# Performance work log

Hardware: AMD Instinct MI355X
Metric: run time of the kernel (lower is better)

The kernel has to match this reference:

```python
import jax, jax.numpy as jnp
import numpy as np

B, L, T = 32, 512, 400
EMB, PRE, ENC, ARNN, DRNN, NSYM = 512, 256, 512, 1024, 1024, 256
MEAN_COEFF, SCALE_COEFF = 1.0, 10.0


def setup_inputs() -> dict:
    key = jax.random.key(0)
    ks = jax.random.split(key, 20)
    s = 0.02
    inp = {
        'memory': jax.random.normal(ks[0], (B, L, ENC), jnp.float32),
        'decoder_inputs': jax.random.normal(ks[1], (B, EMB, T), jnp.float32),
        'memory_lengths': jax.random.randint(ks[2], (B,), L // 2, L + 1).astype(jnp.int64),
        # prenet
        'pW1': jax.random.normal(ks[3], (PRE, EMB), jnp.float32) * s,
        'pb1': jnp.zeros((PRE,), jnp.float32),
        'pW2': jax.random.normal(ks[4], (PRE, PRE), jnp.float32) * s,
        'pb2': jnp.zeros((PRE,), jnp.float32),
        # attention LSTMCell
        'aWih': jax.random.normal(ks[5], (4 * ARNN, PRE + ENC), jnp.float32) * s,
        'aWhh': jax.random.normal(ks[6], (4 * ARNN, ARNN), jnp.float32) * s,
        'abih': jnp.zeros((4 * ARNN,), jnp.float32),
        'abhh': jnp.zeros((4 * ARNN,), jnp.float32),
        # Gaussian attention param linear (weight zero-init in torch; small here)
        'attWp': jax.random.normal(ks[7], (2, ARNN), jnp.float32) * 0.001,
        'attbp': jnp.zeros((2,), jnp.float32),
        # decoder LSTMCell
        'dWih': jax.random.normal(ks[8], (4 * DRNN, ARNN + ENC), jnp.float32) * s,
        'dWhh': jax.random.normal(ks[9], (4 * DRNN, DRNN), jnp.float32) * s,
        'dbih': jnp.zeros((4 * DRNN,), jnp.float32),
        'dbhh': jnp.zeros((4 * DRNN,), jnp.float32),
        # output linear
        'oW': jax.random.normal(ks[10], (NSYM, DRNN + ENC), jnp.float32) * s,
        'ob': jnp.zeros((NSYM,), jnp.float32),
    }
    return inp


def _lstm_cell(x, h, c, Wih, Whh, bih, bhh):
    g = x @ Wih.T + bih + h @ Whh.T + bhh
    i, f, gg, o = jnp.split(g, 4, axis=-1)
    c = jax.nn.sigmoid(f) * c + jax.nn.sigmoid(i) * jnp.tanh(gg)
    h = jax.nn.sigmoid(o) * jnp.tanh(c)
    return h, c


def _decoder_core(memory, decoder_inputs, memory_lengths,
                  pW1, pb1, pW2, pb2,
                  aWih, aWhh, abih, abhh,
                  attWp, attbp,
                  dWih, dWhh, dbih, dbhh,
                  oW, ob):
    b = memory.shape[0]
    Lm = memory.shape[1]
    # go frame + time-major inputs -> prenet (dropout is identity in eval)
    x = jnp.transpose(decoder_inputs, (2, 0, 1))            # [T, B, EMB]
    x = jnp.concatenate([jnp.zeros((1, b, EMB), x.dtype), x], axis=0)  # [T+1, B, EMB]
    x = jax.nn.relu(x @ pW1.T + pb1)
    x = jax.nn.relu(x @ pW2.T + pb2)                        # [T+1, B, PRE]
    x = x[:T]                                               # loop runs T steps

    lin = jnp.arange(Lm, dtype=memory.dtype)[None, :]       # [1, L]
    pad_mask = lin >= memory_lengths[:, None].astype(memory.dtype)  # [B, L] True at pad

    def step(carry, x_t):
        ah, ac, dh, dc, ctx, mean = carry
        cell_in = jnp.concatenate([x_t, ctx], axis=1)
        ah, ac = _lstm_cell(cell_in, ah, ac, aWih, aWhh, abih, abhh)
        params = ah @ attWp.T + attbp                       # [B, 2]
        mean = mean + jnp.exp(params[:, 0:1]) * MEAN_COEFF  # [B, 1]
        scale = jnp.exp(params[:, 1:2]) * SCALE_COEFF       # [B, 1]
        Z = jnp.sqrt(2.0 * np.pi * scale ** 2)
        w = jnp.exp(-0.5 * (lin - mean) ** 2 / scale ** 2) / Z  # [B, L]
        w = jnp.where(pad_mask, 0.0, w)
        ctx = jnp.einsum('bl,bld->bd', w, memory)           # [B, ENC]
        dec_in = jnp.concatenate([ah, ctx], axis=1)
        dh, dc = _lstm_cell(dec_in, dh, dc, dWih, dWhh, dbih, dbhh)
        out = jnp.concatenate([dh, ctx], axis=1) @ oW.T + ob  # [B, NSYM]
        return (ah, ac, dh, dc, ctx, mean), (out, w, params)

    z = jnp.zeros
    carry0 = (z((b, ARNN)), z((b, ARNN)), z((b, DRNN)), z((b, DRNN)),
              z((b, ENC)), z((b, 1)))
    _, (logits, aligns, ps) = jax.lax.scan(step, carry0, x)
    # time-major -> [B, T, ...]
    return (jnp.transpose(logits, (1, 0, 2)),
            jnp.transpose(aligns, (1, 0, 2)),
            jnp.transpose(ps, (1, 0, 2)))


def reference(memory, decoder_inputs, memory_lengths,
              pW1, pb1, pW2, pb2,
              aWih, aWhh, abih, abhh,
              attWp, attbp,
              dWih, dWhh, dbih, dbhh,
              oW, ob):
    return _decoder_core(memory, decoder_inputs, memory_lengths,
                         pW1, pb1, pW2, pb2,
                         aWih, aWhh, abih, abhh,
                         attWp, attbp,
                         dWih, dWhh, dbih, dbhh,
                         oW, ob)
```

## Files before the change

### kernel.cpp

```cpp
#include <hip/hip_runtime.h>
#include <math.h>

#define Bsz   32
#define Lmem  512
#define Tsteps 400
#define EMBD  512
#define PRE   256
#define ENCD  512
#define ARNN  1024
#define DRNN  1024
#define NSYM  256

typedef _Float16 f16x8 __attribute__((ext_vector_type(8)));
typedef float    f32x4 __attribute__((ext_vector_type(4)));
typedef _Float16 half_t;

template<int KIH, int KHH>
__global__ __launch_bounds__(256) void conv_lstm_w(
    const float* __restrict__ Wih, const float* __restrict__ Whh,
    const float* __restrict__ bih, const float* __restrict__ bhh,
    half_t* __restrict__ Wcat, float* __restrict__ bsum)
{
    constexpr int K = KIH + KHH;
    const int j = blockIdx.x;
    const float* srcA = Wih + (size_t)j * KIH;
    const float* srcB = Whh + (size_t)j * KHH;
    half_t* dst = Wcat + (size_t)j * K;
    for (int k = threadIdx.x; k < KIH; k += 256) dst[k]       = (half_t)srcA[k];
    for (int k = threadIdx.x; k < KHH; k += 256) dst[KIH + k] = (half_t)srcB[k];
    if (threadIdx.x == 0) bsum[j] = bih[j] + bhh[j];
}

__global__ __launch_bounds__(256) void conv_mat(
    const float* __restrict__ src, half_t* __restrict__ dst, int n)
{
    for (int i = blockIdx.x * 256 + threadIdx.x; i < n; i += gridDim.x * 256)
        dst[i] = (half_t)src[i];
}

__global__ __launch_bounds__(256) void prenet_kernel(
    const float* __restrict__ din,
    const float* __restrict__ pW1, const float* __restrict__ pb1,
    const float* __restrict__ pW2, const float* __restrict__ pb2,
    half_t* __restrict__ xpre)
{
    __shared__ float xs[8][EMBD];
    __shared__ float h1s[8][PRE];
    const int tid = threadIdx.x;
    const int row0 = blockIdx.x * 8;

    for (int idx = tid; idx < 8 * EMBD; idx += 256) {
        int r = idx >> 9;
        int e = idx & 511;
        int rid = row0 + r;
        int t = rid >> 5;
        int b = rid & 31;
        float v = 0.f;
        if (t > 0) v = din[(size_t)b * EMBD * Tsteps + (size_t)e * Tsteps + (t - 1)];
        xs[r][e] = v;
    }
    __syncthreads();

    {
        float acc[8] = {0.f,0.f,0.f,0.f,0.f,0.f,0.f,0.f};
        const float* wr = pW1 + (size_t)tid * EMBD;
        for (int e = 0; e < EMBD; e += 4) {
            float4 wv = *(const float4*)(wr + e);
            #pragma unroll
            for (int r = 0; r < 8; ++r) {
                float4 xv = *(const float4*)&xs[r][e];
                acc[r] += wv.x * xv.x + wv.y * xv.y + wv.z * xv.z + wv.w * xv.w;
            }
        }
        float bias = pb1[tid];
        #pragma unroll
        for (int r = 0; r < 8; ++r) h1s[r][tid] = fmaxf(acc[r] + bias, 0.f);
    }
    __syncthreads();

    {
        float acc[8] = {0.f,0.f,0.f,0.f,0.f,0.f,0.f,0.f};
        const float* wr = pW2 + (size_t)tid * PRE;
        for (int e = 0; e < PRE; e += 4) {
            float4 wv = *(const float4*)(wr + e);
            #pragma unroll
            for (int r = 0; r < 8; ++r) {
                float4 xv = *(const float4*)&h1s[r][e];
                acc[r] += wv.x * xv.x + wv.y * xv.y + wv.z * xv.z + wv.w * xv.w;
            }
        }
        float bias = pb2[tid];
        #pragma unroll
        for (int r = 0; r < 8; ++r) {
            int rid = row0 + r;
            int t = rid >> 5;
            int b = rid & 31;
            xpre[(size_t)t * Bsz * PRE + (size_t)b * PRE + tid] =
                (half_t)fmaxf(acc[r] + bias, 0.f);
        }
    }
}

template<int K, int L0, int L1, int L2>
__global__ __launch_bounds__(512) void lstm_mfma_kernel(
    const half_t* __restrict__ Wcat, const float* __restrict__ bsum,
    const half_t* __restrict__ s0, const half_t* __restrict__ s1,
    const half_t* __restrict__ s2,
    float* __restrict__ c_state, half_t* __restrict__ h_out)
{
    const int tid   = threadIdx.x;
    const int wave  = tid >> 6;
    const int lane  = tid & 63;
    const int btile = wave & 1;
    const int kq    = wave >> 1;
    const int u0    = blockIdx.x << 2;
    const int m15   = lane & 15;
    const int kh    = lane >> 4;
    constexpr int KQ = K / 4;
    const int kbase = kq * KQ;
    const int jrow  = (m15 >> 2) * 1024 + u0 + (m15 & 3);
    const int b     = (btile << 4) + m15;

    const half_t* arow = Wcat + (size_t)jrow * K + kbase + (kh << 3);
    f32x4 acc = {0.f, 0.f, 0.f, 0.f};

    #pragma unroll
    for (int ki = 0; ki < KQ; ki += 32) {
        f16x8 av = *(const f16x8*)(arow + ki);
        const int kg = kbase + ki + (kh << 3);
        const half_t* bp = (kg < L0)      ? (s0 + b * L0 + kg)
                         : (kg < L0 + L1) ? (s1 + b * L1 + (kg - L0))
                                          : (s2 + b * L2 + (kg - L0 - L1));
        f16x8 bv = *(const f16x8*)bp;
        acc = __builtin_amdgcn_mfma_f32_16x16x32_f16(av, bv, acc, 0, 0, 0);
    }

    __shared__ float gred[4][2][16][16];
    #pragma unroll
    for (int r = 0; r < 4; ++r)
        gred[kq][btile][(kh << 2) + r][m15] = acc[r];
    __syncthreads();

    if (tid < 128) {
        const int ul = tid >> 5;
        const int bb = tid & 31;
        const int bt = bb >> 4;
        const int n  = bb & 15;
        float g[4];
        #pragma unroll
        for (int gi = 0; gi < 4; ++gi) {
            const int mr = (gi << 2) + ul;
            g[gi] = gred[0][bt][mr][n] + gred[1][bt][mr][n]
                  + gred[2][bt][mr][n] + gred[3][bt][mr][n]
                  + bsum[gi * 1024 + u0 + ul];
        }
        const int idx = bb * 1024 + u0 + ul;
        float co = c_state[idx];
        float si = 1.f / (1.f + expf(-g[0]));
        float sf = 1.f / (1.f + expf(-g[1]));
        float so = 1.f / (1.f + expf(-g[3]));
        float cn = sf * co + si * tanhf(g[2]);
        float hn = so * tanhf(cn);
        c_state[idx] = cn;
        h_out[idx] = (half_t)hn;
    }
}

__global__ __launch_bounds__(512) void out_mfma_kernel(
    const half_t* __restrict__ Wo, const float* __restrict__ ob,
    const half_t* __restrict__ dh, const half_t* __restrict__ ctx,
    float* __restrict__ logits, int t)
{
    const int tid   = threadIdx.x;
    const int wave  = tid >> 6;
    const int lane  = tid & 63;
    const int btile = wave & 1;
    const int kq    = wave >> 1;
    const int m15   = lane & 15;
    const int kh    = lane >> 4;
    constexpr int K  = DRNN + ENCD;
    constexpr int KQ = K / 4;
    const int kbase = kq * KQ;
    const int n0 = blockIdx.x << 4;
    const int b  = (btile << 4) + m15;

    const half_t* arow = Wo + (size_t)(n0 + m15) * K + kbase + (kh << 3);
    f32x4 acc = {0.f, 0.f, 0.f, 0.f};

    #pragma unroll
    for (int ki = 0; ki < KQ; ki += 32) {
        f16x8 av = *(const f16x8*)(arow + ki);
        const int kg = kbase + ki + (kh << 3);
        const half_t* bp = (kg < DRNN) ? (dh + b * DRNN + kg)
                                       : (ctx + b * ENCD + (kg - DRNN));
        f16x8 bv = *(const f16x8*)bp;
        acc = __builtin_amdgcn_mfma_f32_16x16x32_f16(av, bv, acc, 0, 0, 0);
    }

    __shared__ float gred[4][2][16][16];
    #pragma unroll
    for (int r = 0; r < 4; ++r)
        gred[kq][btile][(kh << 2) + r][m15] = acc[r];
    __syncthreads();

    {
        const int m  = tid >> 5;
        const int bb = tid & 31;
        const int bt = bb >> 4;
        const int n  = bb & 15;
        float v = gred[0][bt][m][n] + gred[1][bt][m][n]
                + gred[2][bt][m][n] + gred[3][bt][m][n] + ob[n0 + m];
        logits[(size_t)bb * Tsteps * NSYM + (size_t)t * NSYM + n0 + m] = v;
    }
}

__global__ __launch_bounds__(256) void att_kernel(
    const half_t* __restrict__ ah,
    const float* __restrict__ attWp,
    const float* __restrict__ attbp,
    const int*   __restrict__ mlen,
    const float* __restrict__ memory,
    const float* __restrict__ mean_in,
    float* __restrict__ mean_out,
    half_t* __restrict__ ctx,
    float* __restrict__ aligns_out,
    float* __restrict__ ps_out,
    int t)
{
    const int b = blockIdx.x >> 3;
    const int dt = blockIdx.x & 7;
    const int tid = threadIdx.x;

    float p0 = 0.f, p1 = 0.f;
    for (int k = tid; k < ARNN; k += 256) {
        float a = (float)ah[b * ARNN + k];
        p0 += a * attWp[k];
        p1 += a * attWp[ARNN + k];
    }
    #pragma unroll
    for (int off = 32; off > 0; off >>= 1) {
        p0 += __shfl_down(p0, off, 64);
        p1 += __shfl_down(p1, off, 64);
    }
    __shared__ float wred[4][2];
    __shared__ float bc[2];
    const int wid = tid >> 6;
    if ((tid & 63) == 0) { wred[wid][0] = p0; wred[wid][1] = p1; }
    __syncthreads();
    if (tid == 0) {
        float q0 = wred[0][0] + wred[1][0] + wred[2][0] + wred[3][0] + attbp[0];
        float q1 = wred[0][1] + wred[1][1] + wred[2][1] + wred[3][1] + attbp[1];
        float mn = mean_in[b] + expf(q0) * 1.0f;
        float sc = expf(q1) * 10.0f;
        if (dt == 0) {
            mean_out[b] = mn;
            ps_out[(size_t)b * Tsteps * 2 + (size_t)t * 2 + 0] = q0;
            ps_out[(size_t)b * Tsteps * 2 + (size_t)t * 2 + 1] = q1;
        }
        bc[0] = mn; bc[1] = sc;
    }
    __syncthreads();
    const float mn = bc[0], sc = bc[1];
    const float inv_s = 1.f / sc;
    const float coef = 0.3989422804014327f * inv_s;
    const int len = mlen[b];

    __shared__ float wsh[Lmem];
    for (int l = tid; l < Lmem; l += 256) {
        float z = ((float)l - mn) * inv_s;
        float wv = (l < len) ? expf(-0.5f * z * z) * coef : 0.f;
        wsh[l] = wv;
        if (dt == 0)
            aligns_out[(size_t)b * Tsteps * Lmem + (size_t)t * Lmem + l] = wv;
    }
    __syncthreads();

    int lo = (int)fmaxf(0.f, floorf(mn - 9.f * sc));
    int hi = (int)fminf((float)len, ceilf(mn + 9.f * sc) + 1.f);

    const int d = (dt << 6) + (tid & 63);
    const int lq = tid >> 6;
    const float* mb = memory + (size_t)b * Lmem * ENCD + d;
    float acc = 0.f;
    for (int l = lo + lq; l < hi; l += 4)
        acc += wsh[l] * mb[(size_t)l * ENCD];

    __shared__ float red[4][64];
    red[lq][tid & 63] = acc;
    __syncthreads();
    if (tid < 64)
        ctx[b * ENCD + (dt << 6) + tid] =
            (half_t)(red[0][tid] + red[1][tid] + red[2][tid] + red[3][tid]);
}

extern "C" void kernel_launch(void* const* d_in, const int* in_sizes, int n_in,
                              void* d_out, int out_size, void* d_ws, size_t ws_size,
                              hipStream_t stream)
{
    (void)in_sizes; (void)n_in; (void)out_size; (void)ws_size;
    const float* memory = (const float*)d_in[0];
    const float* din    = (const float*)d_in[1];
    const int*   mlen   = (const int*)d_in[2];
    const float* pW1    = (const float*)d_in[3];
    const float* pb1    = (const float*)d_in[4];
    const float* pW2    = (const float*)d_in[5];
    const float* pb2    = (const float*)d_in[6];
    const float* aWih   = (const float*)d_in[7];
    const float* aWhh   = (const float*)d_in[8];
    const float* abih   = (const float*)d_in[9];
    const float* abhh   = (const float*)d_in[10];
    const float* attWp  = (const float*)d_in[11];
    const float* attbp  = (const float*)d_in[12];
    const float* dWih   = (const float*)d_in[13];
    const float* dWhh   = (const float*)d_in[14];
    const float* dbih   = (const float*)d_in[15];
    const float* dbhh   = (const float*)d_in[16];
    const float* oW     = (const float*)d_in[17];
    const float* ob     = (const float*)d_in[18];

    float* logits = (float*)d_out;
    float* aligns = logits + (size_t)Bsz * Tsteps * NSYM;
    float* ps     = aligns + (size_t)Bsz * Tsteps * Lmem;

    char* base = (char*)d_ws;
    auto alloc = [&](size_t bytes) -> char* {
        char* p = base; base += (bytes + 255) & ~(size_t)255; return p;
    };
    half_t* Wcat_a = (half_t*)alloc((size_t)4096 * 1792 * 2);
    half_t* Wcat_d = (half_t*)alloc((size_t)4096 * 2560 * 2);
    half_t* Wo     = (half_t*)alloc((size_t)NSYM * (DRNN + ENCD) * 2);
    float*  bsum_a = (float*)alloc(4096 * 4);
    float*  bsum_d = (float*)alloc(4096 * 4);
    half_t* xpre   = (half_t*)alloc((size_t)Tsteps * Bsz * PRE * 2);
    half_t* ah0    = (half_t*)alloc(Bsz * ARNN * 2);
    half_t* ah1    = (half_t*)alloc(Bsz * ARNN * 2);
    half_t* dh0    = (half_t*)alloc(Bsz * DRNN * 2);
    half_t* dh1    = (half_t*)alloc(Bsz * DRNN * 2);
    half_t* ctx    = (half_t*)alloc(Bsz * ENCD * 2);
    float*  ac     = (float*)alloc(Bsz * ARNN * 4);
    float*  dc     = (float*)alloc(Bsz * DRNN * 4);
    float*  mean0  = (float*)alloc(Bsz * 4);
    float*  mean1  = (float*)alloc(Bsz * 4);

    hipMemsetAsync(ah0,   0, Bsz * ARNN * 2, stream);
    hipMemsetAsync(dh0,   0, Bsz * DRNN * 2, stream);
    hipMemsetAsync(ctx,   0, Bsz * ENCD * 2, stream);
    hipMemsetAsync(ac,    0, Bsz * ARNN * 4, stream);
    hipMemsetAsync(dc,    0, Bsz * DRNN * 4, stream);
    hipMemsetAsync(mean0, 0, Bsz * 4, stream);

    conv_lstm_w<PRE + ENCD, ARNN><<<4096, 256, 0, stream>>>(
        aWih, aWhh, abih, abhh, Wcat_a, bsum_a);
    conv_lstm_w<ARNN + ENCD, DRNN><<<4096, 256, 0, stream>>>(
        dWih, dWhh, dbih, dbhh, Wcat_d, bsum_d);
    conv_mat<<<768, 256, 0, stream>>>(oW, Wo, NSYM * (DRNN + ENCD));
    prenet_kernel<<<Tsteps * Bsz / 8, 256, 0, stream>>>(din, pW1, pb1, pW2, pb2, xpre);

    for (int t = 0; t < Tsteps; ++t) {
        half_t* ah_in  = (t & 1) ? ah1 : ah0;
        half_t* ah_out = (t & 1) ? ah0 : ah1;
        half_t* dh_in  = (t & 1) ? dh1 : dh0;
        half_t* dh_out = (t & 1) ? dh0 : dh1;
        float* mn_in  = (t & 1) ? mean1 : mean0;
        float* mn_out = (t & 1) ? mean0 : mean1;

        lstm_mfma_kernel<1792, PRE, ENCD, ARNN><<<256, 512, 0, stream>>>(
            Wcat_a, bsum_a, xpre + (size_t)t * Bsz * PRE, ctx, ah_in, ac, ah_out);

        att_kernel<<<256, 256, 0, stream>>>(
            ah_out, attWp, attbp, mlen, memory, mn_in, mn_out, ctx, aligns, ps, t);

        lstm_mfma_kernel<2560, ARNN, ENCD, DRNN><<<256, 512, 0, stream>>>(
            Wcat_d, bsum_d, ah_out, ctx, dh_in, dc, dh_out);

        out_mfma_kernel<<<16, 512, 0, stream>>>(Wo, ob, dh_out, ctx, logits, t);
    }
}
```

Before: 17.51 ms.

## Fuse per-step decoder kernels into one persistent kernel with grid barriers

Replaces the 1600 per-timestep kernel launches with one persistent 256-block kernel that loops over timesteps and separates stages with a hand-rolled atomic grid barrier. Each block keeps its slice of both LSTM weight matrices in registers across all steps, so weights are no longer reloaded from memory every step. The output projection is moved into the attention-LSTM phase, one step lagged, so it needs no barrier of its own. Correctness relies on all 256 blocks being co-resident, and the large register footprint may limit occupancy.

```diff
diff --git a/kernel.cpp b/kernel.cpp
--- a/kernel.cpp
+++ b/kernel.cpp
@@ -101,76 +101,42 @@
     }
 }
 
-template<int K, int L0, int L1, int L2>
-__global__ __launch_bounds__(512) void lstm_mfma_kernel(
-    const half_t* __restrict__ Wcat, const float* __restrict__ bsum,
-    const half_t* __restrict__ s0, const half_t* __restrict__ s1,
-    const half_t* __restrict__ s2,
-    float* __restrict__ c_state, half_t* __restrict__ h_out)
-{
-    const int tid   = threadIdx.x;
-    const int wave  = tid >> 6;
-    const int lane  = tid & 63;
-    const int btile = wave & 1;
-    const int kq    = wave >> 1;
-    const int u0    = blockIdx.x << 2;
-    const int m15   = lane & 15;
-    const int kh    = lane >> 4;
-    constexpr int KQ = K / 4;
-    const int kbase = kq * KQ;
-    const int jrow  = (m15 >> 2) * 1024 + u0 + (m15 & 3);
-    const int b     = (btile << 4) + m15;
-
-    const half_t* arow = Wcat + (size_t)jrow * K + kbase + (kh << 3);
-    f32x4 acc = {0.f, 0.f, 0.f, 0.f};
-
-    #pragma unroll
-    for (int ki = 0; ki < KQ; ki += 32) {
-        f16x8 av = *(const f16x8*)(arow + ki);
-        const int kg = kbase + ki + (kh << 3);
-        const half_t* bp = (kg < L0)      ? (s0 + b * L0 + kg)
-                         : (kg < L0 + L1) ? (s1 + b * L1 + (kg - L0))
-                                          : (s2 + b * L2 + (kg - L0 - L1));
-        f16x8 bv = *(const f16x8*)bp;
-        acc = __builtin_amdgcn_mfma_f32_16x16x32_f16(av, bv, acc, 0, 0, 0);
-    }
-
-    __shared__ float gred[4][2][16][16];
-    #pragma unroll
-    for (int r = 0; r < 4; ++r)
-        gred[kq][btile][(kh << 2) + r][m15] = acc[r];
+__device__ __forceinline__ void gsync(unsigned* cnt, unsigned* gen)
+{
     __syncthreads();
-
-    if (tid < 128) {
-        const int ul = tid >> 5;
-        const int bb = tid & 31;
-        const int bt = bb >> 4;
-        const int n  = bb & 15;
-        float g[4];
-        #pragma unroll
-        for (int gi = 0; gi < 4; ++gi) {
-            const int mr = (gi << 2) + ul;
-            g[gi] = gred[0][bt][mr][n] + gred[1][bt][mr][n]
-                  + gred[2][bt][mr][n] + gred[3][bt][mr][n]
-                  + bsum[gi * 1024 + u0 + ul];
-        }
-        const int idx = bb * 1024 + u0 + ul;
-        float co = c_state[idx];
-        float si = 1.f / (1.f + expf(-g[0]));
-        float sf = 1.f / (1.f + expf(-g[1]));
-        float so = 1.f / (1.f + expf(-g[3]));
-        float cn = sf * co + si * tanhf(g[2]);
-        float hn = so * tanhf(cn);
-        c_state[idx] = cn;
-        h_out[idx] = (half_t)hn;
-    }
-}
-
-__global__ __launch_bounds__(512) void out_mfma_kernel(
+    if (threadIdx.x == 0) {
+        __threadfence();
+        unsigned g = __hip_atomic_load(gen, __ATOMIC_RELAXED, __HIP_MEMORY_SCOPE_AGENT);
+        unsigned a = __hip_atomic_fetch_add(cnt, 1u, __ATOMIC_ACQ_REL, __HIP_MEMORY_SCOPE_AGENT);
+        if (a == 255u) {
+            __hip_atomic_store(cnt, 0u, __ATOMIC_RELAXED, __HIP_MEMORY_SCOPE_AGENT);
+            __hip_atomic_store(gen, g + 1u, __ATOMIC_RELEASE, __HIP_MEMORY_SCOPE_AGENT);
+        } else {
+            while (__hip_atomic_load(gen, __ATOMIC_ACQUIRE, __HIP_MEMORY_SCOPE_AGENT) == g)
+                __builtin_amdgcn_s_sleep(2);
+        }
+        __threadfence();
+    }
+    __syncthreads();
+}
+
+__global__ __launch_bounds__(512, 1) void decoder_persistent(
+    const half_t* __restrict__ Wcat_a, const float* __restrict__ bsum_a,
+    const half_t* __restrict__ Wcat_d, const float* __restrict__ bsum_d,
     const half_t* __restrict__ Wo, const float* __restrict__ ob,
-    const half_t* __restrict__ dh, const half_t* __restrict__ ctx,
-    float* __restrict__ logits, int t)
-{
+    const half_t* __restrict__ xpre,
+    const float* __restrict__ attWp, const float* __restrict__ attbp,
+    const int* __restrict__ mlen, const float* __restrict__ memory,
+    float* __restrict__ ac, float* __restrict__ dc,
+    half_t* __restrict__ ah0, half_t* __restrict__ ah1,
+    half_t* __restrict__ dh0, half_t* __restrict__ dh1,
+    half_t* __restrict__ ctx,
+    float* __restrict__ mean0, float* __restrict__ mean1,
+    float* __restrict__ logits, float* __restrict__ aligns,
+    float* __restrict__ ps,
+    unsigned* cnt, unsigned* gen)
+{
+    const int blk   = blockIdx.x;
     const int tid   = threadIdx.x;
     const int wave  = tid >> 6;
     const int lane  = tid & 63;
@@ -178,119 +144,246 @@
     const int kq    = wave >> 1;
     const int m15   = lane & 15;
     const int kh    = lane >> 4;
-    constexpr int K  = DRNN + ENCD;
-    constexpr int KQ = K / 4;
-    const int kbase = kq * KQ;
-    const int n0 = blockIdx.x << 4;
-    const int b  = (btile << 4) + m15;
-
-    const half_t* arow = Wo + (size_t)(n0 + m15) * K + kbase + (kh << 3);
-    f32x4 acc = {0.f, 0.f, 0.f, 0.f};
-
-    #pragma unroll
-    for (int ki = 0; ki < KQ; ki += 32) {
-        f16x8 av = *(const f16x8*)(arow + ki);
-        const int kg = kbase + ki + (kh << 3);
-        const half_t* bp = (kg < DRNN) ? (dh + b * DRNN + kg)
-                                       : (ctx + b * ENCD + (kg - DRNN));
-        f16x8 bv = *(const f16x8*)bp;
-        acc = __builtin_amdgcn_mfma_f32_16x16x32_f16(av, bv, acc, 0, 0, 0);
+    const int u0    = blk << 2;
+    const int jrow  = (m15 >> 2) * 1024 + u0 + (m15 & 3);
+    const int bb    = (btile << 4) + m15;
+
+    constexpr int KA = PRE + ENCD + ARNN;
+    constexpr int KAQ = KA / 4;
+    constexpr int NMA = KAQ / 32;
+    constexpr int KD = ARNN + ENCD + DRNN;
+    constexpr int KDQ = KD / 4;
+    constexpr int NMD = KDQ / 32;
+
+    f16x8 wA[NMA], wD[NMD];
+    {
+        const half_t* ar = Wcat_a + (size_t)jrow * KA + kq * KAQ + (kh << 3);
+        #pragma unroll
+        for (int i = 0; i < NMA; ++i) wA[i] = *(const f16x8*)(ar + i * 32);
+        const half_t* dr = Wcat_d + (size_t)jrow * KD + kq * KDQ + (kh << 3);
+        #pragma unroll
+        for (int i = 0; i < NMD; ++i) wD[i] = *(const f16x8*)(dr + i * 32);
+    }
+    float bsA[4] = {0.f,0.f,0.f,0.f}, bsD[4] = {0.f,0.f,0.f,0.f};
+    if (tid < 128) {
+        const int ul = tid >> 5;
+        #pragma unroll
+        for (int gi = 0; gi < 4; ++gi) {
+            bsA[gi] = bsum_a[gi * 1024 + u0 + ul];
+            bsD[gi] = bsum_d[gi * 1024 + u0 + ul];
+        }
     }
 
     __shared__ float gred[4][2][16][16];
-    #pragma unroll
-    for (int r = 0; r < 4; ++r)
-        gred[kq][btile][(kh << 2) + r][m15] = acc[r];
-    __syncthreads();
+    __shared__ float lred[16][33];
+    __shared__ float wsh[Lmem];
+    __shared__ float red[8][64];
+    __shared__ float wred8[8][2];
+    __shared__ float bc2[2];
+
+    for (int t = 0; t < Tsteps; ++t) {
+        const half_t* ah_in  = (t & 1) ? ah1 : ah0;
+        half_t*       ah_out = (t & 1) ? ah0 : ah1;
+        const half_t* dh_in  = (t & 1) ? dh1 : dh0;
+        half_t*       dh_out = (t & 1) ? dh0 : dh1;
+        const float*  mn_in  = (t & 1) ? mean1 : mean0;
+        float*        mn_out = (t & 1) ? mean0 : mean1;
+
+        {
+            const half_t* s0 = xpre + (size_t)t * Bsz * PRE;
+            f32x4 acc = {0.f, 0.f, 0.f, 0.f};
+            const int kbase = kq * KAQ;
+            #pragma unroll
+            for (int i = 0; i < NMA; ++i) {
+                const int kg = kbase + i * 32 + (kh << 3);
+                const half_t* bp = (kg < PRE)        ? (s0 + bb * PRE + kg)
+                                 : (kg < PRE + ENCD) ? (ctx + bb * ENCD + (kg - PRE))
+                                                     : (ah_in + bb * ARNN + (kg - PRE - ENCD));
+                f16x8 bv = *(const f16x8*)bp;
+                acc = __builtin_amdgcn_mfma_f32_16x16x32_f16(wA[i], bv, acc, 0, 0, 0);
+            }
+            #pragma unroll
+            for (int r = 0; r < 4; ++r)
+                gred[kq][btile][(kh << 2) + r][m15] = acc[r];
+        }
+        {
+            const int b_o = tid & 31;
+            const int ks  = tid >> 5;
+            const half_t* wrow = Wo + (size_t)blk * (DRNN + ENCD) + ks * 96;
+            float outacc = 0.f;
+            #pragma unroll
+            for (int kk = 0; kk < 96; kk += 8) {
+                const int k = ks * 96 + kk;
+                f16x8 wv = *(const f16x8*)(wrow + kk);
+                const half_t* ap = (k < DRNN) ? (dh_in + b_o * DRNN + k)
+                                              : (ctx + b_o * ENCD + (k - DRNN));
+                f16x8 av = *(const f16x8*)ap;
+                #pragma unroll
+                for (int e = 0; e < 8; ++e)
+                    outacc += (float)wv[e] * (float)av[e];
+            }
+            lred[ks][b_o] = outacc;
+        }
+        __syncthreads();
+        if (tid < 128) {
+            const int ul = tid >> 5;
+            const int bq = tid & 31;
+            const int bt = bq >> 4;
+            const int nn = bq & 15;
+            float g[4];
+            #pragma unroll
+            for (int gi = 0; gi < 4; ++gi) {
+                const int mr = (gi << 2) + ul;
+                g[gi] = gred[0][bt][mr][nn] + gred[1][bt][mr][nn]
+                      + gred[2][bt][mr][nn] + gred[3][bt][mr][nn] + bsA[gi];
+            }
+            const int idx = bq * 1024 + u0 + ul;
+            float co = ac[idx];
+            float si = 1.f / (1.f + expf(-g[0]));
+            float sf = 1.f / (1.f + expf(-g[1]));
+            float so = 1.f / (1.f + expf(-g[3]));
+            float cn = sf * co + si * tanhf(g[2]);
+            ac[idx] = cn;
+            ah_out[idx] = (half_t)(so * tanhf(cn));
+        }
+        if (t > 0 && tid < 32) {
+            float s = 0.f;
+            #pragma unroll
+            for (int q = 0; q < 16; ++q) s += lred[q][tid];
+            logits[(size_t)tid * Tsteps * NSYM + (size_t)(t - 1) * NSYM + blk] =
+                s + ob[blk];
+        }
+        gsync(cnt, gen);
+
+        {
+            const int abt = blk >> 3;
+            const int dt  = blk & 7;
+            float p0 = 0.f, p1 = 0.f;
+            for (int k = tid; k < ARNN; k += 512) {
+                float a = (float)ah_out[abt * ARNN + k];
+                p0 += a * attWp[k];
+                p1 += a * attWp[ARNN + k];
+            }
+            #pragma unroll
+            for (int off = 32; off > 0; off >>= 1) {
+                p0 += __shfl_down(p0, off, 64);
+                p1 += __shfl_down(p1, off, 64);
+            }
+            if (lane == 0) { wred8[wave][0] = p0; wred8[wave][1] = p1; }
+            __syncthreads();
+            if (tid == 0) {
+                float q0 = attbp[0], q1 = attbp[1];
+                #pragma unroll
+                for (int w = 0; w < 8; ++w) { q0 += wred8[w][0]; q1 += wred8[w][1]; }
+                float mn = mn_in[abt] + expf(q0) * 1.0f;
+                float sc = expf(q1) * 10.0f;
+                if (dt == 0) {
+                    mn_out[abt] = mn;
+                    ps[(size_t)abt * Tsteps * 2 + (size_t)t * 2 + 0] = q0;
+                    ps[(size_t)abt * Tsteps * 2 + (size_t)t * 2 + 1] = q1;
+                }
+                bc2[0] = mn; bc2[1] = sc;
+            }
+            __syncthreads();
+            const float mn = bc2[0], sc = bc2[1];
+            const float inv_s = 1.f / sc;
+            const float coef = 0.3989422804014327f * inv_s;
+            const int len = mlen[abt];
+            {
+                float z = ((float)tid - mn) * inv_s;
+                float wv = (tid < len) ? expf(-0.5f * z * z) * coef : 0.f;
+                wsh[tid] = wv;
+                if (dt == 0)
+                    aligns[(size_t)abt * Tsteps * Lmem + (size_t)t * Lmem + tid] = wv;
+            }
+            __syncthreads();
+            int lo = (int)fmaxf(0.f, floorf(mn - 9.f * sc));
+            int hi = (int)fminf((float)len, ceilf(mn + 9.f * sc) + 1.f);
+            const int d  = (dt << 6) + (tid & 63);
+            const int lq = tid >> 6;
+            const float* mb = memory + (size_t)abt * Lmem * ENCD + d;
+            float acc = 0.f;
+            for (int l = lo + lq; l < hi; l += 8)
+                acc += wsh[l] * mb[(size_t)l * ENCD];
+            red[lq][tid & 63] = acc;
+            __syncthreads();
+            if (tid < 64) {
+                float s = 0.f;
+                #pragma unroll
+                for (int q = 0; q < 8; ++q) s += red[q][tid];
+                ctx[abt * ENCD + (dt << 6) + tid] = (half_t)s;
+            }
+        }
+        gsync(cnt, gen);
+
+        {
+            f32x4 acc = {0.f, 0.f, 0.f, 0.f};
+            const int kbase = kq * KDQ;
+            #pragma unroll
+            for (int i = 0; i < NMD; ++i) {
+                const int kg = kbase + i * 32 + (kh << 3);
+                const half_t* bp = (kg < ARNN)        ? (ah_out + bb * ARNN + kg)
+                                 : (kg < ARNN + ENCD) ? (ctx + bb * ENCD + (kg - ARNN))
+                                                      : (dh_in + bb * DRNN + (kg - ARNN - ENCD));
+                f16x8 bv = *(const f16x8*)bp;
+                acc = __builtin_amdgcn_mfma_f32_16x16x32_f16(wD[i], bv, acc, 0, 0, 0);
+            }
+            #pragma unroll
+            for (int r = 0; r < 4; ++r)
+                gred[kq][btile][(kh << 2) + r][m15] = acc[r];
+        }
+        __syncthreads();
+        if (tid < 128) {
+            const int ul = tid >> 5;
+            const int bq = tid & 31;
+            const int bt = bq >> 4;
+            const int nn = bq & 15;
+            float g[4];
+            #pragma unroll
+            for (int gi = 0; gi < 4; ++gi) {
+                const int mr = (gi << 2) + ul;
+                g[gi] = gred[0][bt][mr][nn] + gred[1][bt][mr][nn]
+                      + gred[2][bt][mr][nn] + gred[3][bt][mr][nn] + bsD[gi];
+            }
+            const int idx = bq * 1024 + u0 + ul;
+            float co = dc[idx];
+            float si = 1.f / (1.f + expf(-g[0]));
+            float sf = 1.f / (1.f + expf(-g[1]));
+            float so = 1.f / (1.f + expf(-g[3]));
+            float cn = sf * co + si * tanhf(g[2]);
+            dc[idx] = cn;
+            dh_out[idx] = (half_t)(so * tanhf(cn));
+        }
+        gsync(cnt, gen);
+    }
 
     {
-        const int m  = tid >> 5;
-        const int bb = tid & 31;
-        const int bt = bb >> 4;
-        const int n  = bb & 15;
-        float v = gred[0][bt][m][n] + gred[1][bt][m][n]
-                + gred[2][bt][m][n] + gred[3][bt][m][n] + ob[n0 + m];
-        logits[(size_t)bb * Tsteps * NSYM + (size_t)t * NSYM + n0 + m] = v;
-    }
-}
-
-__global__ __launch_bounds__(256) void att_kernel(
-    const half_t* __restrict__ ah,
-    const float* __restrict__ attWp,
-    const float* __restrict__ attbp,
-    const int*   __restrict__ mlen,
-    const float* __restrict__ memory,
-    const float* __restrict__ mean_in,
-    float* __restrict__ mean_out,
-    half_t* __restrict__ ctx,
-    float* __restrict__ aligns_out,
-    float* __restrict__ ps_out,
-    int t)
-{
-    const int b = blockIdx.x >> 3;
-    const int dt = blockIdx.x & 7;
-    const int tid = threadIdx.x;
-
-    float p0 = 0.f, p1 = 0.f;
-    for (int k = tid; k < ARNN; k += 256) {
-        float a = (float)ah[b * ARNN + k];
-        p0 += a * attWp[k];
-        p1 += a * attWp[ARNN + k];
-    }
-    #pragma unroll
-    for (int off = 32; off > 0; off >>= 1) {
-        p0 += __shfl_down(p0, off, 64);
-        p1 += __shfl_down(p1, off, 64);
-    }
-    __shared__ float wred[4][2];
-    __shared__ float bc[2];
-    const int wid = tid >> 6;
-    if ((tid & 63) == 0) { wred[wid][0] = p0; wred[wid][1] = p1; }
-    __syncthreads();
-    if (tid == 0) {
-        float q0 = wred[0][0] + wred[1][0] + wred[2][0] + wred[3][0] + attbp[0];
-        float q1 = wred[0][1] + wred[1][1] + wred[2][1] + wred[3][1] + attbp[1];
-        float mn = mean_in[b] + expf(q0) * 1.0f;
-        float sc = expf(q1) * 10.0f;
-        if (dt == 0) {
-            mean_out[b] = mn;
-            ps_out[(size_t)b * Tsteps * 2 + (size_t)t * 2 + 0] = q0;
-            ps_out[(size_t)b * Tsteps * 2 + (size_t)t * 2 + 1] = q1;
-        }
-        bc[0] = mn; bc[1] = sc;
-    }
-    __syncthreads();
-    const float mn = bc[0], sc = bc[1];
-    const float inv_s = 1.f / sc;
-    const float coef = 0.3989422804014327f * inv_s;
-    const int len = mlen[b];
-
-    __shared__ float wsh[Lmem];
-    for (int l = tid; l < Lmem; l += 256) {
-        float z = ((float)l - mn) * inv_s;
-        float wv = (l < len) ? expf(-0.5f * z * z) * coef : 0.f;
-        wsh[l] = wv;
-        if (dt == 0)
-            aligns_out[(size_t)b * Tsteps * Lmem + (size_t)t * Lmem + l] = wv;
-    }
-    __syncthreads();
-
-    int lo = (int)fmaxf(0.f, floorf(mn - 9.f * sc));
-    int hi = (int)fminf((float)len, ceilf(mn + 9.f * sc) + 1.f);
-
-    const int d = (dt << 6) + (tid & 63);
-    const int lq = tid >> 6;
-    const float* mb = memory + (size_t)b * Lmem * ENCD + d;
-    float acc = 0.f;
-    for (int l = lo + lq; l < hi; l += 4)
-        acc += wsh[l] * mb[(size_t)l * ENCD];
-
-    __shared__ float red[4][64];
-    red[lq][tid & 63] = acc;
-    __syncthreads();
-    if (tid < 64)
-        ctx[b * ENCD + (dt << 6) + tid] =
-            (half_t)(red[0][tid] + red[1][tid] + red[2][tid] + red[3][tid]);
+        const half_t* dhF = ((Tsteps - 1) & 1) ? dh0 : dh1;
+        const int b_o = tid & 31;
+        const int ks  = tid >> 5;
+        const half_t* wrow = Wo + (size_t)blk * (DRNN + ENCD) + ks * 96;
+        float outacc = 0.f;
+        #pragma unroll
+        for (int kk = 0; kk < 96; kk += 8) {
+            const int k = ks * 96 + kk;
+            f16x8 wv = *(const f16x8*)(wrow + kk);
+            const half_t* ap = (k < DRNN) ? (dhF + b_o * DRNN + k)
+                                          : (ctx + b_o * ENCD + (k - DRNN));
+            f16x8 av = *(const f16x8*)ap;
+            #pragma unroll
+            for (int e = 0; e < 8; ++e)
+                outacc += (float)wv[e] * (float)av[e];
+        }
+        lred[ks][b_o] = outacc;
+        __syncthreads();
+        if (tid < 32) {
+            float s = 0.f;
+            #pragma unroll
+            for (int q = 0; q < 16; ++q) s += lred[q][tid];
+            logits[(size_t)tid * Tsteps * NSYM + (size_t)(Tsteps - 1) * NSYM + blk] =
+                s + ob[blk];
+        }
+    }
 }
 
 extern "C" void kernel_launch(void* const* d_in, const int* in_sizes, int n_in,
@@ -341,6 +434,7 @@
     float*  dc     = (float*)alloc(Bsz * DRNN * 4);
     float*  mean0  = (float*)alloc(Bsz * 4);
     float*  mean1  = (float*)alloc(Bsz * 4);
+    unsigned* bar  = (unsigned*)alloc(256);
 
     hipMemsetAsync(ah0,   0, Bsz * ARNN * 2, stream);
     hipMemsetAsync(dh0,   0, Bsz * DRNN * 2, stream);
@@ -348,6 +442,7 @@
     hipMemsetAsync(ac,    0, Bsz * ARNN * 4, stream);
     hipMemsetAsync(dc,    0, Bsz * DRNN * 4, stream);
     hipMemsetAsync(mean0, 0, Bsz * 4, stream);
+    hipMemsetAsync(bar,   0, 256, stream);
 
     conv_lstm_w<PRE + ENCD, ARNN><<<4096, 256, 0, stream>>>(
         aWih, aWhh, abih, abhh, Wcat_a, bsum_a);
@@ -356,23 +451,10 @@
     conv_mat<<<768, 256, 0, stream>>>(oW, Wo, NSYM * (DRNN + ENCD));
     prenet_kernel<<<Tsteps * Bsz / 8, 256, 0, stream>>>(din, pW1, pb1, pW2, pb2, xpre);
 
-    for (int t = 0; t < Tsteps; ++t) {
-        half_t* ah_in  = (t & 1) ? ah1 : ah0;
-        half_t* ah_out = (t & 1) ? ah0 : ah1;
-        half_t* dh_in  = (t & 1) ? dh1 : dh0;
-        half_t* dh_out = (t & 1) ? dh0 : dh1;
-        float* mn_in  = (t & 1) ? mean1 : mean0;
-        float* mn_out = (t & 1) ? mean0 : mean1;
-
-        lstm_mfma_kernel<1792, PRE, ENCD, ARNN><<<256, 512, 0, stream>>>(
-            Wcat_a, bsum_a, xpre + (size_t)t * Bsz * PRE, ctx, ah_in, ac, ah_out);
-
-        att_kernel<<<256, 256, 0, stream>>>(
-            ah_out, attWp, attbp, mlen, memory, mn_in, mn_out, ctx, aligns, ps, t);
-
-        lstm_mfma_kernel<2560, ARNN, ENCD, DRNN><<<256, 512, 0, stream>>>(
-            Wcat_d, bsum_d, ah_out, ctx, dh_in, dc, dh_out);
-
-        out_mfma_kernel<<<16, 512, 0, stream>>>(Wo, ob, dh_out, ctx, logits, t);
-    }
-}
+    decoder_persistent<<<256, 512, 0, stream>>>(
+        Wcat_a, bsum_a, Wcat_d, bsum_d, Wo, ob, xpre,
+        attWp, attbp, mlen, memory,
+        ac, dc, ah0, ah1, dh0, dh1, ctx, mean0, mean1,
+        logits, aligns, ps,
+        bar + 0, bar + 8);
+}
```

Result: slower. 62.08 ms (+254.6%).
